# Kernel optimization log

Measured on AMD Instinct MI355X. Metric: run time of the kernel, lower is better.

## Reference

```python
import jax, jax.numpy as jnp
import numpy as np

SEQ, D_IN, D_OUT, RANK, N_ADAPTERS = 8192, 4096, 4096, 16, 8


def setup_inputs() -> dict:
    key = jax.random.key(0)
    ks = jax.random.split(key, 7)
    return {
        "x": jax.random.normal(ks[0], (SEQ, D_IN), jnp.float32),
        "weight": jax.random.normal(ks[1], (D_IN, D_OUT), jnp.float32) * (D_IN ** -0.5),
        "bias": jax.random.normal(ks[2], (D_OUT,), jnp.float32),
        "A_buffer": jax.random.normal(ks[3], (N_ADAPTERS, RANK, D_IN), jnp.float32) * (D_IN ** -0.5),
        "B_buffer": jax.random.normal(ks[4], (N_ADAPTERS, D_OUT, RANK), jnp.float32) * (RANK ** -0.5),
        "scalings": jax.random.uniform(ks[5], (SEQ,), jnp.float32, 0.5, 2.0),
        "token_indices": jax.random.randint(ks[6], (SEQ,), 0, N_ADAPTERS, jnp.int32),
    }


def reference(x, weight, bias, A_buffer, B_buffer, scalings, token_indices):
    # Base linear layer: [S, D_in] @ [D_in, D_out] + bias
    base_output = x @ weight + bias
    n_adapters = A_buffer.shape[0]
    delta = jnp.zeros_like(base_output)
    # Grouped LoRA GEMM: per-adapter small GEMMs, masked scatter back per token.
    for e in range(n_adapters):
        # run_lora_a_gemm: x @ A[e]^T with per-token scaling -> [S, rank]
        a_out = (x @ A_buffer[e].T) * scalings[:, None]
        # run_lora_b_gemm: a_out @ B[e]^T -> [S, D_out]
        b_out = a_out @ B_buffer[e].T
        delta = delta + jnp.where((token_indices == e)[:, None], b_out, 0.0)
    return base_output + delta
```

## Files before the change

kernel.cpp:

```cpp
#include <hip/hip_runtime.h>
#include <hip/hip_bf16.h>
#include <cstdint>

#define SEQ   8192
#define DIN   4096
#define DOUT  4096
#define RANK  16
#define NAD   8
#define KC    (DIN + NAD*RANK)

using f32x4  = __attribute__((ext_vector_type(4))) float;
using bf16x8 = __attribute__((ext_vector_type(8))) short;

__device__ __forceinline__ unsigned short f2bf(float f) {
  union { float f; uint32_t u; } v; v.f = f;
  return (unsigned short)((v.u + 0x7fffu + ((v.u >> 16) & 1u)) >> 16);
}

__device__ __forceinline__ void async_copy16(void* lds, const void* gmem) {
  __builtin_amdgcn_global_load_lds(
      (__attribute__((address_space(1))) void*)(uintptr_t)gmem,
      (__attribute__((address_space(3))) void*)(uint32_t)(uintptr_t)lds,
      16, 0, 0);
}


__global__ void cvt_x_kernel(const float* __restrict__ x, unsigned short* __restrict__ xcat) {
  const int64_t nchunks = (int64_t)SEQ * DIN / 8;
  for (int64_t c = (int64_t)blockIdx.x * blockDim.x + threadIdx.x; c < nchunks;
       c += (int64_t)gridDim.x * blockDim.x) {
    int64_t base = c * 8;
    int s = (int)(base >> 12);
    int k = (int)(base & (DIN - 1));
    float4 p = *(const float4*)(x + base);
    float4 q = *(const float4*)(x + base + 4);
    union { unsigned short h[8]; int4 v; } o;
    o.h[0]=f2bf(p.x); o.h[1]=f2bf(p.y); o.h[2]=f2bf(p.z); o.h[3]=f2bf(p.w);
    o.h[4]=f2bf(q.x); o.h[5]=f2bf(q.y); o.h[6]=f2bf(q.z); o.h[7]=f2bf(q.w);
    *(int4*)(xcat + (int64_t)s * KC + k) = o.v;
  }
}

__global__ void cvt_a_kernel(const float* __restrict__ a, unsigned short* __restrict__ abf) {
  int c = blockIdx.x * 256 + threadIdx.x;
  int64_t base = (int64_t)c * 8;
  float4 p = *(const float4*)(a + base);
  float4 q = *(const float4*)(a + base + 4);
  union { unsigned short h[8]; int4 v; } o;
  o.h[0]=f2bf(p.x); o.h[1]=f2bf(p.y); o.h[2]=f2bf(p.z); o.h[3]=f2bf(p.w);
  o.h[4]=f2bf(q.x); o.h[5]=f2bf(q.y); o.h[6]=f2bf(q.z); o.h[7]=f2bf(q.w);
  *(int4*)(abf + base) = o.v;
}

__global__ void cvt_w_kernel(const float* __restrict__ w, unsigned short* __restrict__ wcat) {
  int t  = threadIdx.x;
  int bn = blockIdx.x & 127;
  int bk = blockIdx.x >> 7;
  int n = bn * 32 + (t & 31);
  int k = bk * 64 + (t >> 5) * 8;
  union { unsigned short h[8]; int4 v; } o;
#pragma unroll
  for (int j = 0; j < 8; j++)
    o.h[j] = f2bf(w[(int64_t)(k + j) * DOUT + n]);
  *(int4*)(wcat + (int64_t)n * KC + k) = o.v;
}

__global__ void cvt_b_kernel(const float* __restrict__ Bbuf, unsigned short* __restrict__ wcat) {
  int idx = blockIdx.x * 256 + threadIdx.x;
  int n = idx >> 7, er = idx & 127;
  int e = er >> 4, r = er & 15;
  float v = Bbuf[((int64_t)e * DOUT + n) * RANK + r];
  wcat[(int64_t)n * KC + DIN + er] = f2bf(v);
}

__global__ __launch_bounds__(256) void gemm_lora_a(
    const unsigned short* __restrict__ A,
    const unsigned short* __restrict__ Bb,
    float* __restrict__ aout) {
  constexpr int BK = 64;
  __shared__ unsigned short sA[64 * BK];
  __shared__ unsigned short sB[128 * BK];
  int tid = threadIdx.x, wave = tid >> 6, lane = tid & 63;
  int quad = lane >> 4, l16 = lane & 15;
  int mb = blockIdx.x & 127;
  int sp = blockIdx.x >> 7;
  int row0 = mb * 64;
  int kbase = sp * (DIN / 2);
  int wm = wave >> 1, wn = wave & 1;
  int f8 = l16 & 7;

  const f32x4 zero = {0.f, 0.f, 0.f, 0.f};
  f32x4 acc[2][4];
#pragma unroll
  for (int i = 0; i < 2; i++)
#pragma unroll
    for (int j = 0; j < 4; j++) acc[i][j] = zero;

  for (int kt = 0; kt < (DIN / 2) / BK; ++kt) {
    int k0 = kbase + kt * BK;
#pragma unroll
    for (int i = 0; i < 2; i++) {
      int c = i * 256 + tid;
      int r = c >> 3, kc = ((c & 7) ^ (r & 7)) * 8;
      async_copy16(&sA[c * 8], A + (int64_t)(row0 + r) * KC + k0 + kc);
    }
#pragma unroll
    for (int i = 0; i < 4; i++) {
      int c = i * 256 + tid;
      int r = c >> 3, kc = ((c & 7) ^ (r & 7)) * 8;
      async_copy16(&sB[c * 8], Bb + (int64_t)r * DIN + k0 + kc);
    }
    __syncthreads();
#pragma unroll
    for (int ks = 0; ks < 2; ks++) {
      bf16x8 af[2], bfr[4];
      int qq = ks * 4 + quad;
      int qp = (qq ^ f8) * 8;
#pragma unroll
      for (int mi = 0; mi < 2; mi++)
        af[mi] = *(const bf16x8*)&sA[(wm * 32 + mi * 16 + l16) * BK + qp];
#pragma unroll
      for (int ni = 0; ni < 4; ni++)
        bfr[ni] = *(const bf16x8*)&sB[(wn * 64 + ni * 16 + l16) * BK + qp];
#pragma unroll
      for (int mi = 0; mi < 2; mi++)
#pragma unroll
        for (int ni = 0; ni < 4; ni++)
          acc[mi][ni] = __builtin_amdgcn_mfma_f32_16x16x32_bf16(af[mi], bfr[ni], acc[mi][ni], 0, 0, 0);
    }
    __syncthreads();
  }

  float* op = aout + (int64_t)sp * SEQ * 128;
#pragma unroll
  for (int ni = 0; ni < 4; ni++) {
    int er = wn * 64 + ni * 16 + l16;
#pragma unroll
    for (int mi = 0; mi < 2; mi++) {
      int s0 = row0 + wm * 32 + mi * 16 + quad * 4;
#pragma unroll
      for (int r = 0; r < 4; r++)
        op[(int64_t)(s0 + r) * 128 + er] = acc[mi][ni][r];
    }
  }
}

__global__ void lora_combine(const float* __restrict__ aout, const float* __restrict__ scal,
                             const int* __restrict__ tok, unsigned short* __restrict__ xcat) {
  int idx = blockIdx.x * 256 + threadIdx.x;
  int s = idx >> 7, er = idx & 127;
  float v = aout[idx] + aout[idx + (int64_t)SEQ * 128];
  v *= scal[s];
  v = ((er >> 4) == tok[s]) ? v : 0.0f;
  xcat[(int64_t)s * KC + DIN + er] = f2bf(v);
}

__global__ __launch_bounds__(256) void gemm_main(
    const unsigned short* __restrict__ A,
    const unsigned short* __restrict__ B,
    const float* __restrict__ bias,
    float* __restrict__ out) {
  constexpr int BK = 32;
  constexpr int KITERS = KC / BK;
  __shared__ unsigned short sA[128 * BK];
  __shared__ unsigned short sB[128 * BK];
  int tid = threadIdx.x, wave = tid >> 6, lane = tid & 63;
  int quad = lane >> 4, l16 = lane & 15;
  int bn = blockIdx.x & 31, bm = blockIdx.x >> 5;
  int row0 = bm * 128, col0 = bn * 128;
  int wm = wave >> 1, wn = wave & 1;
  int fR = (l16 + (l16 >> 2)) & 3;
  int qp = (quad ^ fR) * 8;

  const f32x4 zero = {0.f, 0.f, 0.f, 0.f};
  f32x4 acc[4][4];
#pragma unroll
  for (int i = 0; i < 4; i++)
#pragma unroll
    for (int j = 0; j < 4; j++) acc[i][j] = zero;

  const unsigned short* Ab = A + (int64_t)row0 * KC;
  const unsigned short* Bb = B + (int64_t)col0 * KC;

  for (int kt = 0; kt < KITERS; ++kt) {
    int k0 = kt * BK;
#pragma unroll
    for (int i = 0; i < 2; i++) {
      int c = i * 256 + tid;
      int r = c >> 2;
      int kc = ((c & 3) ^ ((r + (r >> 2)) & 3)) * 8;
      async_copy16(&sA[c * 8], Ab + (int64_t)r * KC + k0 + kc);
      async_copy16(&sB[c * 8], Bb + (int64_t)r * KC + k0 + kc);
    }
    __syncthreads();
    bf16x8 af[4], bfr[4];
#pragma unroll
    for (int mi = 0; mi < 4; mi++)
      af[mi] = *(const bf16x8*)&sA[(wm * 64 + mi * 16 + l16) * BK + qp];
#pragma unroll
    for (int ni = 0; ni < 4; ni++)
      bfr[ni] = *(const bf16x8*)&sB[(wn * 64 + ni * 16 + l16) * BK + qp];
#pragma unroll
    for (int mi = 0; mi < 4; mi++)
#pragma unroll
      for (int ni = 0; ni < 4; ni++)
        acc[mi][ni] = __builtin_amdgcn_mfma_f32_16x16x32_bf16(af[mi], bfr[ni], acc[mi][ni], 0, 0, 0);
    __syncthreads();
  }

#pragma unroll
  for (int ni = 0; ni < 4; ni++) {
    int col = col0 + wn * 64 + ni * 16 + l16;
    float bv = bias[col];
#pragma unroll
    for (int mi = 0; mi < 4; mi++) {
      int rbase = row0 + wm * 64 + mi * 16 + quad * 4;
#pragma unroll
      for (int r = 0; r < 4; r++)
        out[(int64_t)(rbase + r) * DOUT + col] = acc[mi][ni][r] + bv;
    }
  }
}

__global__ void fb_aout(const float* __restrict__ x, const float* __restrict__ Abuf,
                        const float* __restrict__ scal, const int* __restrict__ tok,
                        float* __restrict__ aout) {
  int s = blockIdx.x;
  int e = tok[s];
  __shared__ float red[256];
  for (int r = 0; r < RANK; ++r) {
    float p = 0.f;
    for (int k = threadIdx.x; k < DIN; k += 256)
      p += x[(int64_t)s * DIN + k] * Abuf[((int64_t)e * RANK + r) * DIN + k];
    red[threadIdx.x] = p;
    __syncthreads();
    for (int off = 128; off > 0; off >>= 1) {
      if (threadIdx.x < off) red[threadIdx.x] += red[threadIdx.x + off];
      __syncthreads();
    }
    if (threadIdx.x == 0) aout[s * RANK + r] = red[0] * scal[s];
    __syncthreads();
  }
}
__global__ void fb_out(const float* __restrict__ x, const float* __restrict__ w,
                       const float* __restrict__ bias, const float* __restrict__ Bbuf,
                       const int* __restrict__ tok, const float* __restrict__ aout,
                       float* __restrict__ out) {
  int64_t idx = (int64_t)blockIdx.x * blockDim.x + threadIdx.x;
  int s = (int)(idx >> 12), n = (int)(idx & (DOUT - 1));
  float accv = bias[n];
  for (int k = 0; k < DIN; ++k)
    accv += x[(int64_t)s * DIN + k] * w[(int64_t)k * DOUT + n];
  int e = tok[s];
  float d = 0.f;
  for (int r = 0; r < RANK; ++r)
    d += aout[s * RANK + r] * Bbuf[((int64_t)e * DOUT + n) * RANK + r];
  out[idx] = accv + d;
}

extern "C" void kernel_launch(void* const* d_in, const int* in_sizes, int n_in,
                              void* d_out, int out_size, void* d_ws, size_t ws_size,
                              hipStream_t stream) {
  const float* x    = (const float*)d_in[0];
  const float* w    = (const float*)d_in[1];
  const float* bias = (const float*)d_in[2];
  const float* Abuf = (const float*)d_in[3];
  const float* Bbuf = (const float*)d_in[4];
  const float* scal = (const float*)d_in[5];
  const int*   tok  = (const int*)d_in[6];
  float* out = (float*)d_out;

  const size_t xcat_b = (size_t)SEQ * KC * 2;
  const size_t wcat_b = (size_t)DOUT * KC * 2;
  const size_t abf_b  = (size_t)NAD * RANK * DIN * 2;
  const size_t aout_b = (size_t)2 * SEQ * 128 * 4;

  if (ws_size >= xcat_b + wcat_b + abf_b + aout_b) {
    unsigned short* xcat = (unsigned short*)d_ws;
    unsigned short* wcat = (unsigned short*)((char*)d_ws + xcat_b);
    unsigned short* abf  = (unsigned short*)((char*)d_ws + xcat_b + wcat_b);
    float*          aout = (float*)((char*)d_ws + xcat_b + wcat_b + abf_b);
    cvt_x_kernel<<<4096, 256, 0, stream>>>(x, xcat);
    cvt_w_kernel<<<8192, 256, 0, stream>>>(w, wcat);
    cvt_b_kernel<<<(DOUT * 128) / 256, 256, 0, stream>>>(Bbuf, wcat);
    cvt_a_kernel<<<(NAD * RANK * DIN / 8) / 256, 256, 0, stream>>>(Abuf, abf);
    gemm_lora_a<<<256, 256, 0, stream>>>(xcat, abf, aout);
    lora_combine<<<(SEQ * 128) / 256, 256, 0, stream>>>(aout, scal, tok, xcat);
    gemm_main<<<(SEQ / 128) * (DOUT / 128), 256, 0, stream>>>(xcat, wcat, bias, out);
  } else {
    float* aout = (float*)d_ws;
    fb_aout<<<SEQ, 256, 0, stream>>>(x, Abuf, scal, tok, aout);
    fb_out<<<(int)(((int64_t)SEQ * DOUT) / 256), 256, 0, stream>>>(x, w, bias, Bbuf, tok, aout, out);
  }
}
```

Before: 637.4 us.

## Rewrite main GEMM as 256x256-tile, 8-wave, double-buffered pipelined kernel

Replaces the 128x128, BK=32 main GEMM with a 512-thread kernel computing 256x256 output tiles using BK=64 and two LDS buffers (128 KB dynamic shared memory). Global-to-LDS async copies for the next K slice are interleaved with MFMA quadrants, using explicit vmcnt/lgkmcnt waits, barriers and setprio so memory traffic overlaps compute. It also swizzles LDS columns with an 8-way XOR and remaps block IDs for better L2 locality. The larger tile raises register pressure (128 accumulator regs per lane) and relies on hand-placed waits that must exactly match the copy ordering.

```diff
diff --git a/kernel.cpp b/kernel.cpp
--- a/kernel.cpp
+++ b/kernel.cpp
@@ -155,66 +155,149 @@
   xcat[(int64_t)s * KC + DIN + er] = f2bf(v);
 }
 
-__global__ __launch_bounds__(256) void gemm_main(
+
+#define CFENCE asm volatile("" ::: "memory")
+
+template<int MQ, int NQ>
+__device__ __forceinline__ void ds_loads(const unsigned short* aT, const unsigned short* bT,
+                                         int wm, int wn, int l16, int quad,
+                                         bf16x8 (&af)[4][2], bf16x8 (&bfr)[2][2]) {
+  int f8 = l16 & 7;
+#pragma unroll
+  for (int ks = 0; ks < 2; ks++) {
+    int qp = ((ks * 4 + quad) ^ f8) * 8;
+#pragma unroll
+    for (int mi = 0; mi < 4; mi++)
+      af[mi][ks] = *(const bf16x8*)&aT[(wm * 128 + MQ * 64 + mi * 16 + l16) * 64 + qp];
+#pragma unroll
+    for (int ni = 0; ni < 2; ni++)
+      bfr[ni][ks] = *(const bf16x8*)&bT[(wn * 64 + NQ * 32 + ni * 16 + l16) * 64 + qp];
+  }
+}
+
+template<int MQ, int NQ>
+__device__ __forceinline__ void mfma_quad(f32x4 (&acc)[8][4], bf16x8 (&af)[4][2], bf16x8 (&bfr)[2][2]) {
+  __builtin_amdgcn_s_setprio(1);
+#pragma unroll
+  for (int mi = 0; mi < 4; mi++)
+#pragma unroll
+    for (int ni = 0; ni < 2; ni++)
+#pragma unroll
+      for (int ks = 0; ks < 2; ks++)
+        acc[MQ * 4 + mi][NQ * 2 + ni] = __builtin_amdgcn_mfma_f32_16x16x32_bf16(
+            af[mi][ks], bfr[ni][ks], acc[MQ * 4 + mi][NQ * 2 + ni], 0, 0, 0);
+  __builtin_amdgcn_s_setprio(0);
+}
+
+__device__ __forceinline__ void stage_A(unsigned short* sAb, const unsigned short* Ag,
+                                        int mq, int k0, int tid) {
+  int rr  = tid >> 3;
+  int q8  = (tid & 7) * 8;
+  int qc8 = ((tid & 7) ^ (rr & 7)) * 8;
+  int r0 = mq * 64 + rr;
+  async_copy16(sAb + r0 * 64 + q8, Ag + (int64_t)r0 * KC + k0 + qc8);
+  int r1 = r0 + 128;
+  async_copy16(sAb + r1 * 64 + q8, Ag + (int64_t)r1 * KC + k0 + qc8);
+}
+
+__device__ __forceinline__ void stage_B(unsigned short* sBb, const unsigned short* Bg,
+                                        int nq, int k0, int tid) {
+  int rB  = ((tid >> 3) & 31) | ((tid >> 8) << 6);
+  int q8  = (tid & 7) * 8;
+  int qc8 = ((tid & 7) ^ ((tid >> 3) & 7)) * 8;
+  int r0 = nq * 32 + rB;
+  async_copy16(sBb + r0 * 64 + q8, Bg + (int64_t)r0 * KC + k0 + qc8);
+  int r1 = r0 + 128;
+  async_copy16(sBb + r1 * 64 + q8, Bg + (int64_t)r1 * KC + k0 + qc8);
+}
+
+#define PHASE(MQ, NQ, aT, bT, STAGE_STMT)                        \
+  ds_loads<MQ, NQ>(aT, bT, wm, wn, l16, quad, af, bfr);          \
+  STAGE_STMT;                                                    \
+  CFENCE; __builtin_amdgcn_s_barrier();                          \
+  asm volatile("s_waitcnt lgkmcnt(0)" ::: "memory");             \
+  mfma_quad<MQ, NQ>(acc, af, bfr)
+
+#define ENDPHASE  CFENCE; __builtin_amdgcn_s_barrier(); CFENCE
+
+__global__ __launch_bounds__(512, 2) void gemm_main8(
     const unsigned short* __restrict__ A,
     const unsigned short* __restrict__ B,
     const float* __restrict__ bias,
     float* __restrict__ out) {
-  constexpr int BK = 32;
-  constexpr int KITERS = KC / BK;
-  __shared__ unsigned short sA[128 * BK];
-  __shared__ unsigned short sB[128 * BK];
+  extern __shared__ unsigned short smem[];
+  unsigned short* a0 = smem;
+  unsigned short* b0 = smem + 16384;
+  unsigned short* a1 = smem + 32768;
+  unsigned short* b1 = smem + 49152;
+
   int tid = threadIdx.x, wave = tid >> 6, lane = tid & 63;
   int quad = lane >> 4, l16 = lane & 15;
-  int bn = blockIdx.x & 31, bm = blockIdx.x >> 5;
-  int row0 = bm * 128, col0 = bn * 128;
-  int wm = wave >> 1, wn = wave & 1;
-  int fR = (l16 + (l16 >> 2)) & 3;
-  int qp = (quad ^ fR) * 8;
+  int wm = wave >> 2, wn = wave & 3;
+
+  int bid = blockIdx.x;
+  int cid = (bid & 7) * 64 + (bid >> 3);
+  int bm = cid >> 4, bn = cid & 15;
+  int row0 = bm * 256, col0 = bn * 256;
+
+  const unsigned short* Ag = A + (int64_t)row0 * KC;
+  const unsigned short* Bg = B + (int64_t)col0 * KC;
 
   const f32x4 zero = {0.f, 0.f, 0.f, 0.f};
-  f32x4 acc[4][4];
-#pragma unroll
-  for (int i = 0; i < 4; i++)
+  f32x4 acc[8][4];
+#pragma unroll
+  for (int i = 0; i < 8; i++)
 #pragma unroll
     for (int j = 0; j < 4; j++) acc[i][j] = zero;
 
-  const unsigned short* Ab = A + (int64_t)row0 * KC;
-  const unsigned short* Bb = B + (int64_t)col0 * KC;
-
-  for (int kt = 0; kt < KITERS; ++kt) {
-    int k0 = kt * BK;
-#pragma unroll
-    for (int i = 0; i < 2; i++) {
-      int c = i * 256 + tid;
-      int r = c >> 2;
-      int kc = ((c & 3) ^ ((r + (r >> 2)) & 3)) * 8;
-      async_copy16(&sA[c * 8], Ab + (int64_t)r * KC + k0 + kc);
-      async_copy16(&sB[c * 8], Bb + (int64_t)r * KC + k0 + kc);
-    }
-    __syncthreads();
-    bf16x8 af[4], bfr[4];
-#pragma unroll
-    for (int mi = 0; mi < 4; mi++)
-      af[mi] = *(const bf16x8*)&sA[(wm * 64 + mi * 16 + l16) * BK + qp];
-#pragma unroll
-    for (int ni = 0; ni < 4; ni++)
-      bfr[ni] = *(const bf16x8*)&sB[(wn * 64 + ni * 16 + l16) * BK + qp];
-#pragma unroll
-    for (int mi = 0; mi < 4; mi++)
-#pragma unroll
-      for (int ni = 0; ni < 4; ni++)
-        acc[mi][ni] = __builtin_amdgcn_mfma_f32_16x16x32_bf16(af[mi], bfr[ni], acc[mi][ni], 0, 0, 0);
-    __syncthreads();
-  }
+  bf16x8 af[4][2], bfr[2][2];
+
+  stage_A(a0, Ag, 0, 0, tid);
+  stage_B(b0, Bg, 0, 0, tid);
+  stage_A(a0, Ag, 1, 0, tid);
+  stage_B(b0, Bg, 1, 0, tid);
+  stage_A(a1, Ag, 0, 64, tid);
+  stage_B(b1, Bg, 0, 64, tid);
+  asm volatile("s_waitcnt vmcnt(4)" ::: "memory");
+  ENDPHASE;
+
+  for (int tp = 0; tp < 32; ++tp) {
+    int kE  = tp * 128;
+    int kO  = kE + 64;
+    int kE2 = kE + 128;
+    int kO2 = kE + 192;
+    PHASE(0, 0, a0, b0, stage_A(a1, Ag, 1, kO,  tid)); ENDPHASE;
+    PHASE(0, 1, a0, b0, stage_B(b1, Bg, 1, kO,  tid)); ENDPHASE;
+    PHASE(1, 0, a0, b0, stage_A(a0, Ag, 0, kE2, tid)); ENDPHASE;
+    PHASE(1, 1, a0, b0, stage_B(b0, Bg, 0, kE2, tid));
+    asm volatile("s_waitcnt vmcnt(4)" ::: "memory");
+    ENDPHASE;
+    PHASE(0, 0, a1, b1, stage_A(a0, Ag, 1, kE2, tid)); ENDPHASE;
+    PHASE(0, 1, a1, b1, stage_B(b0, Bg, 1, kE2, tid)); ENDPHASE;
+    PHASE(1, 0, a1, b1, stage_A(a1, Ag, 0, kO2, tid)); ENDPHASE;
+    PHASE(1, 1, a1, b1, stage_B(b1, Bg, 0, kO2, tid));
+    asm volatile("s_waitcnt vmcnt(4)" ::: "memory");
+    ENDPHASE;
+  }
+
+  PHASE(0, 0, a0, b0, stage_A(a1, Ag, 1, 4160, tid)); ENDPHASE;
+  PHASE(0, 1, a0, b0, stage_B(b1, Bg, 1, 4160, tid)); ENDPHASE;
+  PHASE(1, 0, a0, b0, ((void)0)); ENDPHASE;
+  PHASE(1, 1, a0, b0, ((void)0));
+  asm volatile("s_waitcnt vmcnt(0)" ::: "memory");
+  ENDPHASE;
+  PHASE(0, 0, a1, b1, ((void)0)); ENDPHASE;
+  PHASE(0, 1, a1, b1, ((void)0)); ENDPHASE;
+  PHASE(1, 0, a1, b1, ((void)0)); ENDPHASE;
+  PHASE(1, 1, a1, b1, ((void)0));
 
 #pragma unroll
   for (int ni = 0; ni < 4; ni++) {
     int col = col0 + wn * 64 + ni * 16 + l16;
     float bv = bias[col];
 #pragma unroll
-    for (int mi = 0; mi < 4; mi++) {
-      int rbase = row0 + wm * 64 + mi * 16 + quad * 4;
+    for (int mi = 0; mi < 8; mi++) {
+      int rbase = row0 + wm * 128 + mi * 16 + quad * 4;
 #pragma unroll
       for (int r = 0; r < 4; r++)
         out[(int64_t)(rbase + r) * DOUT + col] = acc[mi][ni][r] + bv;
@@ -276,6 +359,12 @@
   const size_t aout_b = (size_t)2 * SEQ * 128 * 4;
 
   if (ws_size >= xcat_b + wcat_b + abf_b + aout_b) {
+    static bool lds_attr_done = false;
+    if (!lds_attr_done) {
+      (void)hipFuncSetAttribute((const void*)gemm_main8,
+                                hipFuncAttributeMaxDynamicSharedMemorySize, 131072);
+      lds_attr_done = true;
+    }
     unsigned short* xcat = (unsigned short*)d_ws;
     unsigned short* wcat = (unsigned short*)((char*)d_ws + xcat_b);
     unsigned short* abf  = (unsigned short*)((char*)d_ws + xcat_b + wcat_b);
@@ -286,7 +375,7 @@
     cvt_a_kernel<<<(NAD * RANK * DIN / 8) / 256, 256, 0, stream>>>(Abuf, abf);
     gemm_lora_a<<<256, 256, 0, stream>>>(xcat, abf, aout);
     lora_combine<<<(SEQ * 128) / 256, 256, 0, stream>>>(aout, scal, tok, xcat);
-    gemm_main<<<(SEQ / 128) * (DOUT / 128), 256, 0, stream>>>(xcat, wcat, bias, out);
+    gemm_main8<<<512, 512, 131072, stream>>>(xcat, wcat, bias, out);
   } else {
     float* aout = (float*)d_ws;
     fb_aout<<<SEQ, 256, 0, stream>>>(x, Abuf, scal, tok, aout);
```

Result: faster. 579.8 us (-9.0%).
